# Performance work log

Hardware: AMD Instinct MI355X
Metric: run time of the kernel (lower is better)

Reference implementation:

```python
import jax, jax.numpy as jnp
import numpy as np
import math

FILTER_SIZE = 11
FILTER_SIGMA = 1.5
C1 = 0.01 ** 2
C2 = 0.03 ** 2
PAD = FILTER_SIZE // 2


def _make_gauss_kernel(sigma, kernel_size, channel=3):
    mean = np.floor(0.5 * kernel_size)
    x = np.arange(kernel_size, dtype=np.float64)
    k1d = np.exp(-((x - mean) ** 2) / (2 * sigma ** 2)) * (1.0 / (2 * math.pi * sigma ** 2))
    k2d = np.outer(k1d, k1d).astype(np.float32)
    k2d = k2d / k2d.sum()
    # OIHW depthwise kernel: [channel, 1, k, k]
    return np.broadcast_to(k2d[None, None], (channel, 1, kernel_size, kernel_size)).copy()


def _depthwise_blur(x, kernel):
    # x: [B, 3, H, W], kernel: [3, 1, k, k]; groups=3, SAME padding (k//2)
    return jax.lax.conv_general_dilated(
        x, kernel,
        window_strides=(1, 1),
        padding=[(PAD, PAD), (PAD, PAD)],
        dimension_numbers=('NCHW', 'OIHW', 'NCHW'),
        feature_group_count=3,
    )


def setup_inputs() -> dict:
    key = jax.random.key(0)
    k1, k2 = jax.random.split(key)
    B, C, H, W = 32, 3, 512, 512
    image1 = jax.random.uniform(k1, (B, C, H, W), dtype=jnp.float32)
    image2 = jax.random.uniform(k2, (B, C, H, W), dtype=jnp.float32)
    gauss_kernel = jnp.asarray(_make_gauss_kernel(FILTER_SIGMA, FILTER_SIZE, channel=3))
    return {"image1": image1, "image2": image2, "gauss_kernel": gauss_kernel}


def reference(image1, image2, gauss_kernel):
    mu1 = _depthwise_blur(image1, gauss_kernel)
    mu2 = _depthwise_blur(image2, gauss_kernel)
    mu1_sq = mu1 * mu1
    mu2_sq = mu2 * mu2
    mu1_mu2 = mu1 * mu2
    sig1_sq = _depthwise_blur(image1 * image1, gauss_kernel) - mu1_sq
    sig2_sq = _depthwise_blur(image2 * image2, gauss_kernel) - mu2_sq
    sig1_sig2 = _depthwise_blur(image1 * image2, gauss_kernel) - mu1_mu2
    ssim_num = (2.0 * mu1_mu2 + C1) * (2.0 * sig1_sig2 + C2)
    ssim_den = (mu1_sq + mu2_sq + C1) * (sig1_sq + sig2_sq + C2)
    ssim_map = ssim_num / ssim_den
    dssim_map = (1.0 - ssim_map) * 0.5
    return dssim_map.mean()  # size_average=True
```

## Files before the change

### kernel.cpp

```cpp
#include <hip/hip_runtime.h>
#include <math.h>


namespace {
constexpr int IMG = 512;
constexpr int TW = 32;
constexpr int RB = 64;
constexpr int RING = RB + 10;
constexpr int SLOT = 44;
constexpr int XGN = TW / 8;
constexpr int NCHUNK = IMG / RB;
constexpr int CTILES = IMG / TW;
constexpr int NIMG = 96;
constexpr float C1c = 1e-4f;
constexpr float C2c = 9e-4f;
constexpr float INV_N = 1.0f / 25165824.0f;
}

typedef float v2f __attribute__((ext_vector_type(2)));

__global__ void dssim_zero(float* ws) { ws[0] = 0.0f; }

__global__ void dssim_final(const float* __restrict__ ws, float* __restrict__ out) {
  out[0] = ws[0] * INV_N;
}

__global__ __launch_bounds__(256, 3) void dssim_main(
    const float* __restrict__ im1, const float* __restrict__ im2,
    const float* __restrict__ gk, float* __restrict__ ws)
{
  __shared__ float sR[XGN * RING * SLOT];

  const int tid = threadIdx.x;
  const int bid = blockIdx.x;
  const int img = bid >> 4;
  const int tsx = bid & 15;
  const int X0s = tsx * TW;

  const float* __restrict__ p1 = im1 + (size_t)img * (IMG * IMG);
  const float* __restrict__ p2 = im2 + (size_t)img * (IMG * IMG);

  float wt[11];
  {
    float ic = 1.0f / sqrtf(gk[5 * 11 + 5]);
    #pragma unroll
    for (int i = 0; i < 11; ++i) wt[i] = gk[i * 11 + 5] * ic;
  }
  v2f wp[12];
  #pragma unroll
  for (int m = 0; m < 12; ++m) {
    float lo = (m <= 10) ? wt[m] : 0.f;
    float hi = (m >= 1) ? wt[m - 1] : 0.f;
    wp[m].x = lo; wp[m].y = hi;
  }

  const int c   = tid & 31;
  const int yg  = tid >> 5;
  const int xg3 = c >> 3;
  const int cl  = c & 7;

  float lsum = 0.f;

  for (int k = 0; k < NCHUNK; ++k) {
    const int r0    = (k == 0) ? -5 : RB * k + 5;
    const int ntask = (k == 0) ? XGN * RING : XGN * RB;
    for (int t = tid; t < ntask; t += 256) {
      const int xg = t & 3, dr = t >> 2;
      const int r  = r0 + dr;
      const int rr = (r + 5) % RING;
      const int cb = X0s + xg * 8 - 8;

      float a24[24], b24[24];
      if ((unsigned)r < (unsigned)IMG) {
        const float* row1 = p1 + r * IMG;
        const float* row2 = p2 + r * IMG;
        if (cb >= 0 && cb + 24 <= IMG) {
          #pragma unroll
          for (int i = 0; i < 6; ++i) {
            float4 v1 = *(const float4*)(row1 + cb + 4 * i);
            float4 v2 = *(const float4*)(row2 + cb + 4 * i);
            a24[4*i+0] = v1.x; a24[4*i+1] = v1.y; a24[4*i+2] = v1.z; a24[4*i+3] = v1.w;
            b24[4*i+0] = v2.x; b24[4*i+1] = v2.y; b24[4*i+2] = v2.z; b24[4*i+3] = v2.w;
          }
        } else {
          #pragma unroll
          for (int e = 0; e < 24; ++e) {
            int cc = cb + e;
            bool ok = (unsigned)cc < (unsigned)IMG;
            a24[e] = ok ? row1[cc] : 0.f;
            b24[e] = ok ? row2[cc] : 0.f;
          }
        }
      } else {
        #pragma unroll
        for (int e = 0; e < 24; ++e) { a24[e] = 0.f; b24[e] = 0.f; }
      }

      v2f o0[4], o1[4], o2[4], o3[4], o4[4];
      #pragma unroll
      for (int jp = 0; jp < 4; ++jp) {
        o0[jp] = 0.f; o1[jp] = 0.f; o2[jp] = 0.f; o3[jp] = 0.f; o4[jp] = 0.f;
      }
      #pragma unroll
      for (int e = 0; e < 18; ++e) {
        float va = a24[e + 3], vb = b24[e + 3];
        float pa = va * va, pb = vb * vb, pab = va * vb;
        v2f va2; va2.x = va; va2.y = va;
        v2f vb2; vb2.x = vb; vb2.y = vb;
        v2f pa2; pa2.x = pa; pa2.y = pa;
        v2f pb2; pb2.x = pb; pb2.y = pb;
        v2f pc2; pc2.x = pab; pc2.y = pab;
        #pragma unroll
        for (int jp = 0; jp < 4; ++jp) {
          int m = e - 2 * jp;
          if (m >= 0 && m < 12) {
            v2f w = wp[m];
            o0[jp] = __builtin_elementwise_fma(w, va2, o0[jp]);
            o1[jp] = __builtin_elementwise_fma(w, vb2, o1[jp]);
            o2[jp] = __builtin_elementwise_fma(w, pa2, o2[jp]);
            o3[jp] = __builtin_elementwise_fma(w, pb2, o3[jp]);
            o4[jp] = __builtin_elementwise_fma(w, pc2, o4[jp]);
          }
        }
      }

      const int base = (xg * RING + rr) * SLOT;
      #pragma unroll
      for (int jp = 0; jp < 4; ++jp) {
        *(float4*)&sR[base + 8 * jp]     = make_float4(o0[jp].x, o1[jp].x, o2[jp].x, o3[jp].x);
        *(float4*)&sR[base + 8 * jp + 4] = make_float4(o0[jp].y, o1[jp].y, o2[jp].y, o3[jp].y);
      }
      *(float4*)&sR[base + 32] = make_float4(o4[0].x, o4[0].y, o4[1].x, o4[1].y);
      *(float4*)&sR[base + 36] = make_float4(o4[2].x, o4[2].y, o4[3].x, o4[3].y);
    }
    __syncthreads();

    v2f m1p[4], m2p[4], e11p[4], e22p[4], e12p[4];
    #pragma unroll
    for (int jp = 0; jp < 4; ++jp) {
      m1p[jp] = 0.f; m2p[jp] = 0.f; e11p[jp] = 0.f; e22p[jp] = 0.f; e12p[jp] = 0.f;
    }

    const int rbase = (RB * k + yg * 8) % RING;
    #pragma unroll
    for (int rr = 0; rr < 18; ++rr) {
      int idx = rbase + rr;
      if (idx >= RING) idx -= RING;
      const int a = (xg3 * RING + idx) * SLOT;
      float4 v4 = *(const float4*)&sR[a + 4 * cl];
      float  v5 = sR[a + 32 + cl];
      v2f x1; x1.x = v4.x; x1.y = v4.x;
      v2f x2; x2.x = v4.y; x2.y = v4.y;
      v2f x3; x3.x = v4.z; x3.y = v4.z;
      v2f x4; x4.x = v4.w; x4.y = v4.w;
      v2f x5; x5.x = v5;   x5.y = v5;
      #pragma unroll
      for (int jp = 0; jp < 4; ++jp) {
        int m = rr - 2 * jp;
        if (m >= 0 && m < 12) {
          v2f w = wp[m];
          m1p[jp]  = __builtin_elementwise_fma(w, x1, m1p[jp]);
          m2p[jp]  = __builtin_elementwise_fma(w, x2, m2p[jp]);
          e11p[jp] = __builtin_elementwise_fma(w, x3, e11p[jp]);
          e22p[jp] = __builtin_elementwise_fma(w, x4, e22p[jp]);
          e12p[jp] = __builtin_elementwise_fma(w, x5, e12p[jp]);
        }
      }
    }

    #pragma unroll
    for (int jp = 0; jp < 4; ++jp) {
      v2f m1 = m1p[jp], m2 = m2p[jp];
      v2f m1s = m1 * m1, m2s = m2 * m2, m12 = m1 * m2;
      v2f s11 = e11p[jp] - m1s, s22 = e22p[jp] - m2s, s12 = e12p[jp] - m12;
      v2f num = (2.f * m12 + C1c) * (2.f * s12 + C2c);
      v2f den = (m1s + m2s + C1c) * (s11 + s22 + C2c);
      lsum += (1.f - num.x * __builtin_amdgcn_rcpf(den.x)) * 0.5f;
      lsum += (1.f - num.y * __builtin_amdgcn_rcpf(den.y)) * 0.5f;
    }
    __syncthreads();
  }

  #pragma unroll
  for (int off = 32; off > 0; off >>= 1) lsum += __shfl_down(lsum, off);
  if ((tid & 63) == 0) atomicAdd(ws, lsum);
}

extern "C" void kernel_launch(void* const* d_in, const int* in_sizes, int n_in,
                              void* d_out, int out_size, void* d_ws, size_t ws_size,
                              hipStream_t stream) {
  const float* im1 = (const float*)d_in[0];
  const float* im2 = (const float*)d_in[1];
  const float* gk  = (const float*)d_in[2];
  float* out = (float*)d_out;
  float* ws  = (float*)d_ws;

  hipLaunchKernelGGL(dssim_zero, dim3(1), dim3(1), 0, stream, ws);
  hipLaunchKernelGGL(dssim_main, dim3(NIMG * CTILES), dim3(256), 0, stream,
                     im1, im2, gk, ws);
  hipLaunchKernelGGL(dssim_final, dim3(1), dim3(1), 0, stream, ws, out);
}
```

Before: 293.0 us.

## Store horizontal blur intermediates as fp16 in LDS and raise occupancy

The five horizontally blurred channels (mu1, mu2, E11, E22, E12) are packed into half-precision pairs in shared memory instead of fp32. That cuts the per-block LDS footprint from about 52KB to about 28KB, and launch bounds are raised from 3 to 5 blocks per SM to use the freed space. The goal is more resident waves to hide LDS and global load latency, plus less LDS traffic. The cost is pack/unpack conversions and fp16 rounding in the intermediates, which feed a variance computed by subtraction (E[x^2]-mu^2), so accuracy may degrade. Register pressure from the tighter launch bound could also cause spills.

```diff
diff --git a/kernel.cpp b/kernel.cpp
--- a/kernel.cpp
+++ b/kernel.cpp
@@ -1,4 +1,5 @@
 #include <hip/hip_runtime.h>
+#include <hip/hip_fp16.h>
 #include <math.h>
 
 
@@ -7,7 +8,8 @@
 constexpr int TW = 32;
 constexpr int RB = 64;
 constexpr int RING = RB + 10;
-constexpr int SLOT = 44;
+constexpr int SLOT_AB = 10;
+constexpr int SLOT_C  = 8;
 constexpr int XGN = TW / 8;
 constexpr int NCHUNK = IMG / RB;
 constexpr int CTILES = IMG / TW;
@@ -19,17 +21,22 @@
 
 typedef float v2f __attribute__((ext_vector_type(2)));
 
+#define PACK2(lo, hi) \
+  ((unsigned)__half_as_ushort(__float2half_rn(lo)) | \
+   ((unsigned)__half_as_ushort(__float2half_rn(hi)) << 16))
+
 __global__ void dssim_zero(float* ws) { ws[0] = 0.0f; }
 
 __global__ void dssim_final(const float* __restrict__ ws, float* __restrict__ out) {
   out[0] = ws[0] * INV_N;
 }
 
-__global__ __launch_bounds__(256, 3) void dssim_main(
+__global__ __launch_bounds__(256, 5) void dssim_main(
     const float* __restrict__ im1, const float* __restrict__ im2,
     const float* __restrict__ gk, float* __restrict__ ws)
 {
-  __shared__ float sR[XGN * RING * SLOT];
+  __shared__ uint2          sAB[XGN * RING * SLOT_AB];
+  __shared__ unsigned short sC [XGN * RING * SLOT_C];
 
   const int tid = threadIdx.x;
   const int bid = blockIdx.x;
@@ -124,14 +131,23 @@
         }
       }
 
-      const int base = (xg * RING + rr) * SLOT;
+      const int baseAB = (xg * RING + rr) * SLOT_AB;
       #pragma unroll
       for (int jp = 0; jp < 4; ++jp) {
-        *(float4*)&sR[base + 8 * jp]     = make_float4(o0[jp].x, o1[jp].x, o2[jp].x, o3[jp].x);
-        *(float4*)&sR[base + 8 * jp + 4] = make_float4(o0[jp].y, o1[jp].y, o2[jp].y, o3[jp].y);
-      }
-      *(float4*)&sR[base + 32] = make_float4(o4[0].x, o4[0].y, o4[1].x, o4[1].y);
-      *(float4*)&sR[base + 36] = make_float4(o4[2].x, o4[2].y, o4[3].x, o4[3].y);
+        unsigned u0x = PACK2(o0[jp].x, o1[jp].x);
+        unsigned u0y = PACK2(o2[jp].x, o3[jp].x);
+        unsigned u1x = PACK2(o0[jp].y, o1[jp].y);
+        unsigned u1y = PACK2(o2[jp].y, o3[jp].y);
+        *(uint4*)&sAB[baseAB + 2 * jp] = make_uint4(u0x, u0y, u1x, u1y);
+      }
+      const int baseC = (xg * RING + rr) * SLOT_C;
+      {
+        unsigned w0 = PACK2(o4[0].x, o4[0].y);
+        unsigned w1 = PACK2(o4[1].x, o4[1].y);
+        unsigned w2 = PACK2(o4[2].x, o4[2].y);
+        unsigned w3 = PACK2(o4[3].x, o4[3].y);
+        *(uint4*)&sC[baseC] = make_uint4(w0, w1, w2, w3);
+      }
     }
     __syncthreads();
 
@@ -146,14 +162,18 @@
     for (int rr = 0; rr < 18; ++rr) {
       int idx = rbase + rr;
       if (idx >= RING) idx -= RING;
-      const int a = (xg3 * RING + idx) * SLOT;
-      float4 v4 = *(const float4*)&sR[a + 4 * cl];
-      float  v5 = sR[a + 32 + cl];
-      v2f x1; x1.x = v4.x; x1.y = v4.x;
-      v2f x2; x2.x = v4.y; x2.y = v4.y;
-      v2f x3; x3.x = v4.z; x3.y = v4.z;
-      v2f x4; x4.x = v4.w; x4.y = v4.w;
-      v2f x5; x5.x = v5;   x5.y = v5;
+      uint2 vab = sAB[(xg3 * RING + idx) * SLOT_AB + cl];
+      unsigned short uc = sC[(xg3 * RING + idx) * SLOT_C + cl];
+      __half2 hmu = *(const __half2*)&vab.x;
+      __half2 hee = *(const __half2*)&vab.y;
+      float f1 = __low2float(hmu), f2 = __high2float(hmu);
+      float f3 = __low2float(hee), f4 = __high2float(hee);
+      float f5 = __half2float(__ushort_as_half(uc));
+      v2f x1; x1.x = f1; x1.y = f1;
+      v2f x2; x2.x = f2; x2.y = f2;
+      v2f x3; x3.x = f3; x3.y = f3;
+      v2f x4; x4.x = f4; x4.y = f4;
+      v2f x5; x5.x = f5; x5.y = f5;
       #pragma unroll
       for (int jp = 0; jp < 4; ++jp) {
         int m = rr - 2 * jp;
```

Result: slower. 426.7 us (+45.6%).
